# Kernel optimization log

Measured on AMD Instinct MI355X. Metric: run time of the kernel, lower is better.

Reference implementation:

```python
import jax, jax.numpy as jnp
import numpy as np

V = 8000; TZ = 128; TU = 256; B = 64; H = 1024; E = 512; DG = 64
GI = E + 2 * H + DG  # GRU input size = embed + z_ctx + u_ctx + degree


def _build_sparse_z(rng):
    # faithful vectorized version of get_sparse_selective_input (minus vocab SLOT branch)
    z_np = rng.integers(0, V + 10, size=(TZ, B))  # some ids >= V -> OOV copy path
    res = np.full((TZ, B, V + TZ), 1e-10, np.float32)
    w = z_np[:-1]                                   # [TZ-1, B]
    cond = (w == 2) | (w >= V)
    ti, bi = np.meshgrid(np.arange(TZ - 1), np.arange(B), indexing='ij')
    col = np.where(cond, V + ti, w)
    val = np.where(cond, np.float32(5.0), np.float32(1.0))
    res[ti + 1, bi, col] = val
    return jnp.asarray(res.transpose(1, 0, 2))      # [B, TZ, V+TZ]


def setup_inputs():
    key = jax.random.key(0)
    ks = jax.random.split(key, 16)
    s = 0.02
    iv = 1.0 / np.sqrt(H)
    return dict(
        z_enc_out=jax.random.normal(ks[0], (TZ, B, H), jnp.float32),
        u_enc_out=jax.random.normal(ks[1], (TU, B, H), jnp.float32),
        m_t_input=jax.random.randint(ks[2], (1, B), 0, V),
        degree_input=jax.random.normal(ks[3], (B, DG), jnp.float32),
        last_hidden=jax.random.normal(ks[4], (1, B, H), jnp.float32),
        sparse_z_input=_build_sparse_z(np.random.default_rng(0)),
        emb_W=jax.random.normal(ks[5], (V, E), jnp.float32) * s,
        attn_z_W=jax.random.normal(ks[6], (H, 2 * H), jnp.float32) * s,
        attn_z_b=jnp.zeros((H,), jnp.float32),
        attn_z_v=jax.random.normal(ks[7], (H,), jnp.float32) * iv,
        attn_u_W=jax.random.normal(ks[8], (H, 2 * H), jnp.float32) * s,
        attn_u_b=jnp.zeros((H,), jnp.float32),
        attn_u_v=jax.random.normal(ks[9], (H,), jnp.float32) * iv,
        gru_Wih=jax.random.normal(ks[10], (3 * H, GI), jnp.float32) * s,
        gru_Whh=jax.random.normal(ks[11], (3 * H, H), jnp.float32) * s,
        gru_bih=jnp.zeros((3 * H,), jnp.float32),
        gru_bhh=jnp.zeros((3 * H,), jnp.float32),
        proj_W=jax.random.normal(ks[12], (V, 3 * H), jnp.float32) * s,
        proj_b=jnp.zeros((V,), jnp.float32),
        copy2_W=jax.random.normal(ks[13], (H, H), jnp.float32) * s,
        copy2_b=jnp.zeros((H,), jnp.float32),
    )


def _attn(hidden, enc, W, b, v):
    # hidden [1,B,H], enc [T,B,H] -> context [1,B,H] (Bahdanau additive attention)
    enc_b = jnp.transpose(enc, (1, 0, 2))                       # [B,T,H]
    Hrep = jnp.broadcast_to(jnp.transpose(hidden, (1, 0, 2)), enc_b.shape)
    energy = jnp.tanh(jnp.concatenate([Hrep, enc_b], -1) @ W.T + b)  # [B,T,H]
    scores = jnp.einsum('bth,h->bt', energy, v)[:, None, :]    # [B,1,T]
    alpha = jax.nn.softmax(scores, axis=2)
    ctx = jnp.einsum('bit,bth->bih', alpha, enc_b)              # [B,1,H]
    return jnp.transpose(ctx, (1, 0, 2))                        # [1,B,H]


def _gru_step(x, h, Wih, Whh, bih, bhh):
    # single step, torch gate order (r, z, n)
    gi = x @ Wih.T + bih
    gh = h @ Whh.T + bhh
    ir, iz, inn = jnp.split(gi, 3, -1)
    hr, hz, hn = jnp.split(gh, 3, -1)
    r = jax.nn.sigmoid(ir + hr)
    z = jax.nn.sigmoid(iz + hz)
    n = jnp.tanh(inn + r * hn)
    return (1.0 - z) * n + z * h


def reference(z_enc_out, u_enc_out, m_t_input, degree_input, last_hidden,
              sparse_z_input, emb_W, attn_z_W, attn_z_b, attn_z_v,
              attn_u_W, attn_u_b, attn_u_v, gru_Wih, gru_Whh, gru_bih, gru_bhh,
              proj_W, proj_b, copy2_W, copy2_b):
    m_embed = emb_W[m_t_input]                                  # [1,B,E]
    z_ctx = _attn(last_hidden, z_enc_out, attn_z_W, attn_z_b, attn_z_v)  # [1,B,H]
    u_ctx = _attn(last_hidden, u_enc_out, attn_u_W, attn_u_b, attn_u_v)  # [1,B,H]
    gru_in = jnp.concatenate([m_embed, u_ctx, z_ctx, degree_input[None]], axis=2)
    gru_out = _gru_step(gru_in, last_hidden, gru_Wih, gru_Whh, gru_bih, gru_bhh)
    new_hidden = gru_out                                        # single-layer GRU, 1 step
    gen_score = (jnp.concatenate([z_ctx, u_ctx, gru_out], 2) @ proj_W.T + proj_b)[0]  # [B,V]
    # pointer copy scores over z encoder states
    z_cs = jnp.tanh(jnp.transpose(z_enc_out, (1, 0, 2)) @ copy2_W.T + copy2_b)  # [B,TZ,H]
    z_cs = jnp.einsum('bth,bh->bt', z_cs, gru_out[0])           # [B,TZ]
    m = jnp.max(z_cs, axis=1, keepdims=True)
    e = jnp.exp(z_cs - m)
    z_copy = jnp.log(jnp.einsum('bt,btv->bv', e, sparse_z_input)) + m  # [B,V+TZ]
    scores = jax.nn.softmax(jnp.concatenate([gen_score, z_copy], axis=1), axis=1)
    gen_s, zc = scores[:, :V], scores[:, V:]
    proba = jnp.concatenate([gen_s + zc[:, :V], zc[:, V:]], axis=1)  # [B, V+TZ]
    return (proba, new_hidden, gru_out)
```

## Files before the change

kernel.cpp:

```cpp
#include <hip/hip_runtime.h>
#include <cmath>

#define B64 64
#define H 1024
#define E 512
#define DG 64
#define GIN 2624
#define TZ 128
#define TU 256
#define V 8000
#define VT 8128
#define NC 16128

using bf16x8 = __attribute__((ext_vector_type(8))) short;
using f32x4  = __attribute__((ext_vector_type(4))) float;

__device__ inline unsigned pack2(float a, float b) {
    unsigned ua = __float_as_uint(a) + 0x8000u;
    unsigned ub = __float_as_uint(b) + 0x8000u;
    return __builtin_amdgcn_perm(ub, ua, 0x07060302u);
}
__device__ inline uint2 pack4(float4 v) {
    return make_uint2(pack2(v.x, v.y), pack2(v.z, v.w));
}

__device__ inline float fast_tanh(float x) {
    float e = __expf(2.f * x);
    return 1.f - 2.f / (e + 1.f);
}
__device__ inline float fast_sig(float x) {
    return 1.f / (1.f + __expf(-x));
}

__device__ inline void gl_lds16(const void* gptr, void* lptr) {
    __builtin_amdgcn_global_load_lds(
        (const __attribute__((address_space(1))) void*)gptr,
        (__attribute__((address_space(3))) void*)lptr, 16, 0, 0);
}

__global__ void k_cvt_all(const float* __restrict__ u_enc, const float* __restrict__ z_enc,
                          const float* __restrict__ azW, const float* __restrict__ auW,
                          const float* __restrict__ c2W,
                          unsigned short* __restrict__ ubf, unsigned short* __restrict__ zbf,
                          unsigned short* __restrict__ azWbf, unsigned short* __restrict__ auWbf,
                          unsigned short* __restrict__ c2Wbf)
{
    int n = blockIdx.x, k4 = threadIdx.x * 4;
    const float* src; unsigned short* dst; int ld, koff, r;
    if (n < 16384)      { src = u_enc; dst = ubf;   ld = 1024; koff = 0;    r = n; }
    else if (n < 24576) { src = z_enc; dst = zbf;   ld = 1024; koff = 0;    r = n - 16384; }
    else if (n < 25600) { src = azW;   dst = azWbf; ld = 2048; koff = 1024; r = n - 24576; }
    else if (n < 26624) { src = auW;   dst = auWbf; ld = 2048; koff = 1024; r = n - 25600; }
    else                { src = c2W;   dst = c2Wbf; ld = 1024; koff = 0;    r = n - 26624; }
    float4 v = *(const float4*)(src + (size_t)r * ld + koff + k4);
    *(uint2*)(dst + (size_t)r * 1024 + k4) = pack4(v);
}

__global__ __launch_bounds__(256) void fused_tanh_dot_bf(
    const unsigned short* __restrict__ A,
    const unsigned short* __restrict__ W,
    const float* __restrict__ addv, int add_stride,
    const float* __restrict__ multv, int mult_stride,
    float* __restrict__ outs)
{
    __shared__ unsigned short As[128 * 32];
    __shared__ unsigned short Bs[128 * 32];
    const int tid  = threadIdx.x;
    const int wave = tid >> 6, lane = tid & 63;
    const int wm = wave >> 1, wn = wave & 1;
    const int q = lane >> 4, l16 = lane & 15;
    const int m0 = blockIdx.x * 128;
    const int n0 = blockIdx.y * 128;
    const int lrow = lane >> 2;
    const int lk   = (lane & 3) * 8;

    f32x4 acc[4][4];
#pragma unroll
    for (int i = 0; i < 4; ++i)
#pragma unroll
        for (int j = 0; j < 4; ++j) acc[i][j] = f32x4{0.f, 0.f, 0.f, 0.f};

    for (int kt = 0; kt < 32; ++kt) {
        const int k0 = kt * 32;
        __syncthreads();
#pragma unroll
        for (int j = 0; j < 2; ++j) {
            int r0 = (wave * 2 + j) * 16;
            gl_lds16(A + (size_t)(m0 + r0 + lrow) * 1024 + k0 + lk, &As[r0 * 32]);
            gl_lds16(W + (size_t)(n0 + r0 + lrow) * 1024 + k0 + lk, &Bs[r0 * 32]);
        }
        __syncthreads();
        bf16x8 af[4], bfr[4];
#pragma unroll
        for (int t = 0; t < 4; ++t) af[t]  = *(bf16x8*)&As[(wm * 64 + t * 16 + l16) * 32 + q * 8];
#pragma unroll
        for (int t = 0; t < 4; ++t) bfr[t] = *(bf16x8*)&Bs[(wn * 64 + t * 16 + l16) * 32 + q * 8];
#pragma unroll
        for (int tm = 0; tm < 4; ++tm)
#pragma unroll
            for (int tn = 0; tn < 4; ++tn)
                acc[tm][tn] = __builtin_amdgcn_mfma_f32_16x16x32_bf16(
                    af[tm], bfr[tn], acc[tm][tn], 0, 0, 0);
    }

#pragma unroll
    for (int tm = 0; tm < 4; ++tm) {
#pragma unroll
        for (int r = 0; r < 4; ++r) {
            int R = m0 + wm * 64 + tm * 16 + q * 4 + r;
            int b = R & 63;
            float s = 0.f;
#pragma unroll
            for (int tn = 0; tn < 4; ++tn) {
                int col = n0 + wn * 64 + tn * 16 + l16;
                float e = acc[tm][tn][r] + addv[(size_t)b * add_stride + col];
                s += fast_tanh(e) * multv[(size_t)b * mult_stride + col];
            }
            s += __shfl_xor(s, 1);
            s += __shfl_xor(s, 2);
            s += __shfl_xor(s, 4);
            s += __shfl_xor(s, 8);
            if (l16 == 0) atomicAdd(&outs[R], s);
        }
    }
}

__global__ __launch_bounds__(256) void ftd_z_combo(
    const unsigned short* __restrict__ A,
    const unsigned short* __restrict__ Wz,
    const float* __restrict__ hbz, const float* __restrict__ azv,
    float* __restrict__ scores,
    const unsigned short* __restrict__ Wc,
    const float* __restrict__ c2b,
    float* __restrict__ tz)
{
    __shared__ unsigned short As[128 * 32];
    __shared__ unsigned short Bs[128 * 32];
    const int tid  = threadIdx.x;
    const int wave = tid >> 6, lane = tid & 63;
    const int wm = wave >> 1, wn = wave & 1;
    const int q = lane >> 4, l16 = lane & 15;
    const int m0 = blockIdx.x * 128;
    const bool isz = blockIdx.y < 8;
    const int n0 = (isz ? blockIdx.y : blockIdx.y - 8) * 128;
    const unsigned short* W = isz ? Wz : Wc;
    const int lrow = lane >> 2;
    const int lk   = (lane & 3) * 8;

    f32x4 acc[4][4];
#pragma unroll
    for (int i = 0; i < 4; ++i)
#pragma unroll
        for (int j = 0; j < 4; ++j) acc[i][j] = f32x4{0.f, 0.f, 0.f, 0.f};

    for (int kt = 0; kt < 32; ++kt) {
        const int k0 = kt * 32;
        __syncthreads();
#pragma unroll
        for (int j = 0; j < 2; ++j) {
            int r0 = (wave * 2 + j) * 16;
            gl_lds16(A + (size_t)(m0 + r0 + lrow) * 1024 + k0 + lk, &As[r0 * 32]);
            gl_lds16(W + (size_t)(n0 + r0 + lrow) * 1024 + k0 + lk, &Bs[r0 * 32]);
        }
        __syncthreads();
        bf16x8 af[4], bfr[4];
#pragma unroll
        for (int t = 0; t < 4; ++t) af[t]  = *(bf16x8*)&As[(wm * 64 + t * 16 + l16) * 32 + q * 8];
#pragma unroll
        for (int t = 0; t < 4; ++t) bfr[t] = *(bf16x8*)&Bs[(wn * 64 + t * 16 + l16) * 32 + q * 8];
#pragma unroll
        for (int tm = 0; tm < 4; ++tm)
#pragma unroll
            for (int tn = 0; tn < 4; ++tn)
                acc[tm][tn] = __builtin_amdgcn_mfma_f32_16x16x32_bf16(
                    af[tm], bfr[tn], acc[tm][tn], 0, 0, 0);
    }

    if (isz) {
#pragma unroll
        for (int tm = 0; tm < 4; ++tm) {
#pragma unroll
            for (int r = 0; r < 4; ++r) {
                int R = m0 + wm * 64 + tm * 16 + q * 4 + r;
                int b = R & 63;
                float s = 0.f;
#pragma unroll
                for (int tn = 0; tn < 4; ++tn) {
                    int col = n0 + wn * 64 + tn * 16 + l16;
                    float e = acc[tm][tn][r] + hbz[(size_t)b * 1024 + col];
                    s += fast_tanh(e) * azv[col];
                }
                s += __shfl_xor(s, 1);
                s += __shfl_xor(s, 2);
                s += __shfl_xor(s, 4);
                s += __shfl_xor(s, 8);
                if (l16 == 0) atomicAdd(&scores[R], s);
            }
        }
    } else {
#pragma unroll
        for (int tm = 0; tm < 4; ++tm) {
#pragma unroll
            for (int r = 0; r < 4; ++r) {
                int R = m0 + wm * 64 + tm * 16 + q * 4 + r;
#pragma unroll
                for (int tn = 0; tn < 4; ++tn) {
                    int col = n0 + wn * 64 + tn * 16 + l16;
                    tz[(size_t)R * 1024 + col] = fast_tanh(acc[tm][tn][r] + c2b[col]);
                }
            }
        }
    }
}

__global__ __launch_bounds__(256) void gemm_bt_mfma(
    const float* __restrict__ A, int lda,
    const float* __restrict__ W, int ldw, int koff,
    const float* __restrict__ bias,
    float* __restrict__ C, int N,
    int ks_total, int ks_chunk)
{
    __shared__ short As[64][40];
    __shared__ short Bs[64][40];
    const int tid  = threadIdx.x;
    const int wave = tid >> 6, lane = tid & 63;
    const int wm = wave >> 1, wn = wave & 1;
    const int q = lane >> 4, l16 = lane & 15;
    const int n0 = blockIdx.x * 64;
    const int kb = blockIdx.y * ks_chunk;
    const int ke = min(kb + ks_chunk, ks_total);

    f32x4 acc[2][2];
#pragma unroll
    for (int i = 0; i < 2; ++i)
#pragma unroll
        for (int j = 0; j < 2; ++j) acc[i][j] = f32x4{0.f, 0.f, 0.f, 0.f};

    for (int ks = kb; ks < ke; ++ks) {
        const int k0 = ks * 32;
        __syncthreads();
#pragma unroll
        for (int i = 0; i < 2; ++i) {
            int slot = i * 256 + tid;
            int row  = slot >> 3;
            int kq   = (slot & 7) << 2;
            float4 a = *(const float4*)(A + (size_t)row * lda + k0 + kq);
            *(uint2*)&As[row][kq] = pack4(a);
            float4 w = *(const float4*)(W + (size_t)(n0 + row) * ldw + koff + k0 + kq);
            *(uint2*)&Bs[row][kq] = pack4(w);
        }
        __syncthreads();
        bf16x8 af[2], bfr[2];
#pragma unroll
        for (int t = 0; t < 2; ++t) af[t]  = *(bf16x8*)&As[wm * 32 + t * 16 + l16][q * 8];
#pragma unroll
        for (int t = 0; t < 2; ++t) bfr[t] = *(bf16x8*)&Bs[wn * 32 + t * 16 + l16][q * 8];
#pragma unroll
        for (int tm = 0; tm < 2; ++tm)
#pragma unroll
            for (int tn = 0; tn < 2; ++tn)
                acc[tm][tn] = __builtin_amdgcn_mfma_f32_16x16x32_bf16(
                    af[tm], bfr[tn], acc[tm][tn], 0, 0, 0);
    }

#pragma unroll
    for (int tm = 0; tm < 2; ++tm) {
#pragma unroll
        for (int r = 0; r < 4; ++r) {
            int b = wm * 32 + tm * 16 + q * 4 + r;
#pragma unroll
            for (int tn = 0; tn < 2; ++tn) {
                int n = n0 + wn * 32 + tn * 16 + l16;
                float v = acc[tm][tn][r];
                if (blockIdx.y == 0) v += bias[n];
                atomicAdd(&C[(size_t)b * N + n], v);
            }
        }
    }
}

__global__ void k_gather(const int* __restrict__ mt, const float* __restrict__ embW,
                         const float* __restrict__ degree, float* __restrict__ x)
{
    int b = blockIdx.x, tid = threadIdx.x;
    int m = mt[b];
    for (int k = tid; k < E; k += 128) x[(size_t)b * GIN + k] = embW[(size_t)m * E + k];
    if (tid < DG) x[(size_t)b * GIN + E + 2 * H + tid] = degree[b * DG + tid];
}

__global__ __launch_bounds__(256) void k_softmax_ctx_bf(
    const float* __restrict__ scores, const unsigned short* __restrict__ encbf, int T,
    float* __restrict__ x, int xoff, float* __restrict__ y, int yoff)
{
    __shared__ float red[256];
    __shared__ float al[256];
    int b = blockIdx.x, hc = blockIdx.y, tid = threadIdx.x;
    float s = (tid < T) ? scores[tid * B64 + b] : -1e30f;
    red[tid] = s; __syncthreads();
    for (int off = 128; off > 0; off >>= 1) {
        if (tid < off) red[tid] = fmaxf(red[tid], red[tid + off]);
        __syncthreads();
    }
    float mx = red[0]; __syncthreads();
    float e = (tid < T) ? __expf(s - mx) : 0.f;
    red[tid] = e; __syncthreads();
    for (int off = 128; off > 0; off >>= 1) {
        if (tid < off) red[tid] += red[tid + off];
        __syncthreads();
    }
    float inv = 1.f / red[0];
    al[tid] = e * inv;
    __syncthreads();
    int h = hc * 512 + tid * 2;
    float a0 = 0.f, a1 = 0.f;
#pragma unroll 4
    for (int t = 0; t < T; ++t) {
        unsigned u = *(const unsigned*)(encbf + ((size_t)t * B64 + b) * 1024 + h);
        float w = al[t];
        a0 += w * __uint_as_float(u << 16);
        a1 += w * __uint_as_float(u & 0xffff0000u);
    }
    x[(size_t)b * GIN + xoff + h]     = a0;
    x[(size_t)b * GIN + xoff + h + 1] = a1;
    y[(size_t)b * 3072 + yoff + h]     = a0;
    y[(size_t)b * 3072 + yoff + h + 1] = a1;
}

__global__ void k_gate(const float* __restrict__ gi, const float* __restrict__ gh,
                       const float* __restrict__ h0, float* __restrict__ gru,
                       float* __restrict__ y, float* __restrict__ out_hid,
                       float* __restrict__ out_gru)
{
    int b = blockIdx.x, tid = threadIdx.x;
    for (int j = tid; j < H; j += 256) {
        float ir = gi[(size_t)b * 3072 + j];
        float iz = gi[(size_t)b * 3072 + H + j];
        float in_ = gi[(size_t)b * 3072 + 2 * H + j];
        float hr = gh[(size_t)b * 3072 + j];
        float hz = gh[(size_t)b * 3072 + H + j];
        float hn = gh[(size_t)b * 3072 + 2 * H + j];
        float r = fast_sig(ir + hr);
        float z = fast_sig(iz + hz);
        float n = fast_tanh(in_ + r * hn);
        float h = h0[(size_t)b * H + j];
        float o = (1.f - z) * n + z * h;
        gru[(size_t)b * H + j] = o;
        y[(size_t)b * 3072 + 2 * H + j] = o;
        out_hid[(size_t)b * H + j] = o;
        out_gru[(size_t)b * H + j] = o;
    }
}

__global__ __launch_bounds__(512) void k_zcs_dot(
    const float* __restrict__ tz, const float* __restrict__ gru,
    float* __restrict__ zraw)
{
    __shared__ float g[1024];
    int b = blockIdx.x, quarter = blockIdx.y, tid = threadIdx.x;
    int wave = tid >> 6, lane = tid & 63;
    for (int i = tid; i < 1024; i += 512) g[i] = gru[(size_t)b * 1024 + i];
    __syncthreads();
    float gr[16];
#pragma unroll
    for (int j = 0; j < 16; ++j) gr[j] = g[lane * 16 + j];
    int t0 = quarter * 32;
#pragma unroll
    for (int i = 0; i < 4; ++i) {
        int t = t0 + wave + i * 8;
        const float* row = tz + ((size_t)t * B64 + b) * 1024 + lane * 16;
        float s = 0.f;
#pragma unroll
        for (int c = 0; c < 4; ++c) {
            float4 v = *(const float4*)(row + c * 4);
            s += v.x * gr[c * 4 + 0] + v.y * gr[c * 4 + 1]
               + v.z * gr[c * 4 + 2] + v.w * gr[c * 4 + 3];
        }
#pragma unroll
        for (int off = 32; off > 0; off >>= 1) s += __shfl_xor(s, off);
        if (lane == 0) zraw[b * TZ + t] = s;
    }
}

__global__ void k_expw(const float* __restrict__ zraw,
                       float* __restrict__ ew, float* __restrict__ mb)
{
    __shared__ float r2[2];
    int b = blockIdx.x, tid = threadIdx.x;
    float s = zraw[b * TZ + tid];
    float m = s;
#pragma unroll
    for (int off = 32; off > 0; off >>= 1) m = fmaxf(m, __shfl_xor(m, off));
    if ((tid & 63) == 0) r2[tid >> 6] = m;
    __syncthreads();
    m = fmaxf(r2[0], r2[1]);
    ew[b * TZ + tid] = __expf(s - m);
    if (tid == 0) mb[b] = m;
}

__global__ __launch_bounds__(256) void k_sparse(
    const float* __restrict__ sz, const float* __restrict__ ew,
    const float* __restrict__ mb, float* __restrict__ zcopy)
{
    __shared__ float es[TZ];
    int c = blockIdx.x, b = blockIdx.y, tid = threadIdx.x;
    if (tid < TZ) es[tid] = ew[b * TZ + tid];
    __syncthreads();
    if (tid >= 254) return;
    int v4 = c * 254 + tid;
    const f32x4* base = (const f32x4*)(sz + (size_t)b * TZ * VT);
    float4 acc = make_float4(0.f, 0.f, 0.f, 0.f);
#pragma unroll 16
    for (int t = 0; t < TZ; ++t) {
        f32x4 xv = __builtin_nontemporal_load(&base[(size_t)t * (VT / 4) + v4]);
        float e = es[t];
        acc.x += e * xv[0]; acc.y += e * xv[1]; acc.z += e * xv[2]; acc.w += e * xv[3];
    }
    float m = mb[b];
    int v = v4 * 4;
    zcopy[(size_t)b * VT + v + 0] = __logf(acc.x) + m;
    zcopy[(size_t)b * VT + v + 1] = __logf(acc.y) + m;
    zcopy[(size_t)b * VT + v + 2] = __logf(acc.z) + m;
    zcopy[(size_t)b * VT + v + 3] = __logf(acc.w) + m;
}

__global__ __launch_bounds__(1024) void k_final(
    const float* __restrict__ gen, const float* __restrict__ zcopy,
    float* __restrict__ proba)
{
    __shared__ float lg[NC];
    __shared__ float wred[16];
    int b = blockIdx.x, tid = threadIdx.x;
    int lane = tid & 63, wave = tid >> 6;
    for (int i = tid; i < V; i += 1024) lg[i] = gen[(size_t)b * V + i];
    for (int i = tid; i < VT; i += 1024) lg[V + i] = zcopy[(size_t)b * VT + i];
    __syncthreads();
    float mx = -1e30f;
    for (int i = tid; i < NC; i += 1024) mx = fmaxf(mx, lg[i]);
#pragma unroll
    for (int off = 32; off > 0; off >>= 1) mx = fmaxf(mx, __shfl_xor(mx, off));
    if (lane == 0) wred[wave] = mx;
    __syncthreads();
    mx = wred[0];
#pragma unroll
    for (int w = 1; w < 16; ++w) mx = fmaxf(mx, wred[w]);
    __syncthreads();
    float sm = 0.f;
    for (int i = tid; i < NC; i += 1024) sm += __expf(lg[i] - mx);
#pragma unroll
    for (int off = 32; off > 0; off >>= 1) sm += __shfl_xor(sm, off);
    if (lane == 0) wred[wave] = sm;
    __syncthreads();
    float Z = 0.f;
#pragma unroll
    for (int w = 0; w < 16; ++w) Z += wred[w];
    float invZ = 1.f / Z;
    for (int v = tid; v < VT; v += 1024) {
        float p = __expf(lg[V + v] - mx) * invZ;
        if (v < V) p += __expf(lg[v] - mx) * invZ;
        proba[(size_t)b * VT + v] = p;
    }
}

extern "C" void kernel_launch(void* const* d_in, const int* in_sizes, int n_in,
                              void* d_out, int out_size, void* d_ws, size_t ws_size,
                              hipStream_t stream)
{
    const float* z_enc  = (const float*)d_in[0];
    const float* u_enc  = (const float*)d_in[1];
    const int*   mt     = (const int*)d_in[2];
    const float* degree = (const float*)d_in[3];
    const float* h0     = (const float*)d_in[4];
    const float* sz     = (const float*)d_in[5];
    const float* embW   = (const float*)d_in[6];
    const float* azW    = (const float*)d_in[7];
    const float* azb    = (const float*)d_in[8];
    const float* azv    = (const float*)d_in[9];
    const float* auW    = (const float*)d_in[10];
    const float* aub    = (const float*)d_in[11];
    const float* auv    = (const float*)d_in[12];
    const float* Wih    = (const float*)d_in[13];
    const float* Whh    = (const float*)d_in[14];
    const float* bih    = (const float*)d_in[15];
    const float* bhh    = (const float*)d_in[16];
    const float* pW     = (const float*)d_in[17];
    const float* pb     = (const float*)d_in[18];
    const float* c2W    = (const float*)d_in[19];
    const float* c2b    = (const float*)d_in[20];

    float* ws       = (float*)d_ws;
    float* scores_z = ws;
    float* scores_u = ws + 8192;
    float* hbz      = ws + 32768;
    float* hbu      = ws + 98304;
    float* gi       = ws + 163840;
    float* gh       = ws + 360448;
    float* gen      = ws + 557056;
    float* x        = ws + 1069056;
    float* y        = ws + 1236992;
    float* gru      = ws + 1433600;
    float* ew       = ws + 1499136;
    float* mb       = ws + 1507328;
    float* zcopy    = ws + 1507392;
    float* tz       = ws + 2027584;
    unsigned short* ubf   = (unsigned short*)(ws + 2027584 + 8388608);
    unsigned short* zbf   = ubf + (size_t)16384 * 1024;
    unsigned short* azWbf = zbf + (size_t)8192 * 1024;
    unsigned short* auWbf = azWbf + (size_t)1024 * 1024;
    unsigned short* c2Wbf = auWbf + (size_t)1024 * 1024;
    float* zraw = ws + 24571968;

    float* out_proba = (float*)d_out;
    float* out_hid   = out_proba + (size_t)B64 * VT;
    float* out_gru   = out_hid + (size_t)B64 * H;

    hipMemsetAsync(ws, 0, 1069056 * sizeof(float), stream);

    k_cvt_all<<<27648, 256, 0, stream>>>(u_enc, z_enc, azW, auW, c2W,
                                         ubf, zbf, azWbf, auWbf, c2Wbf);

    gemm_bt_mfma<<<dim3(16, 8), 256, 0, stream>>>(h0, 1024, azW, 2048, 0, azb, hbz, 1024, 32, 4);
    gemm_bt_mfma<<<dim3(16, 8), 256, 0, stream>>>(h0, 1024, auW, 2048, 0, aub, hbu, 1024, 32, 4);
    k_gather<<<64, 128, 0, stream>>>(mt, embW, degree, x);
    gemm_bt_mfma<<<dim3(48, 8), 256, 0, stream>>>(h0, 1024, Whh, 1024, 0, bhh, gh, 3072, 32, 4);

    ftd_z_combo<<<dim3(64, 16), 256, 0, stream>>>(zbf, azWbf, hbz, azv, scores_z,
                                                  c2Wbf, c2b, tz);
    fused_tanh_dot_bf<<<dim3(128, 8), 256, 0, stream>>>(ubf, auWbf, hbu, 1024, auv, 0, scores_u);

    k_softmax_ctx_bf<<<dim3(64, 2), 256, 0, stream>>>(scores_z, zbf, TZ, x, 1536, y, 0);
    k_softmax_ctx_bf<<<dim3(64, 2), 256, 0, stream>>>(scores_u, ubf, TU, x, 512, y, 1024);

    gemm_bt_mfma<<<dim3(48, 8), 256, 0, stream>>>(x, GIN, Wih, GIN, 0, bih, gi, 3072, 82, 11);
    k_gate<<<64, 256, 0, stream>>>(gi, gh, h0, gru, y, out_hid, out_gru);

    k_zcs_dot<<<dim3(64, 4), 512, 0, stream>>>(tz, gru, zraw);
    k_expw<<<64, 128, 0, stream>>>(zraw, ew, mb);

    gemm_bt_mfma<<<dim3(125, 8), 256, 0, stream>>>(y, 3072, pW, 3072, 0, pb, gen, 8000, 96, 12);

    k_sparse<<<dim3(8, 64), 256, 0, stream>>>(sz, ew, mb, zcopy);

    k_final<<<64, 1024, 0, stream>>>(gen, zcopy, out_proba);
}
```

Baseline: 806.7 us.

## Merge small kernels into fewer launches across gather, gemms, attention and softmax

Several small kernels are folded together: the embedding gather joins the bf16 conversion kernel, the three hidden-state GEMMs become one launch, the z/u/copy tanh-dot kernels become one grid, both softmax-context calls share one launch, and the exp/max step moves into the sparse kernel. This cuts launch overhead and lets independent work fill the GPU at the same time. In exchange each k_sparse block recomputes the row max and exponentials, and the merged kernels add a little branching.

```diff
diff --git a/kernel.cpp b/kernel.cpp
--- a/kernel.cpp
+++ b/kernel.cpp
@@ -43,9 +43,19 @@
                           const float* __restrict__ c2W,
                           unsigned short* __restrict__ ubf, unsigned short* __restrict__ zbf,
                           unsigned short* __restrict__ azWbf, unsigned short* __restrict__ auWbf,
-                          unsigned short* __restrict__ c2Wbf)
-{
-    int n = blockIdx.x, k4 = threadIdx.x * 4;
+                          unsigned short* __restrict__ c2Wbf,
+                          const int* __restrict__ mt, const float* __restrict__ embW,
+                          const float* __restrict__ degree, float* __restrict__ x)
+{
+    int n = blockIdx.x, tid = threadIdx.x;
+    if (n >= 27648) {
+        int b = n - 27648;
+        int m = mt[b];
+        for (int k = tid; k < E; k += 256) x[(size_t)b * GIN + k] = embW[(size_t)m * E + k];
+        if (tid < DG) x[(size_t)b * GIN + E + 2 * H + tid] = degree[b * DG + tid];
+        return;
+    }
+    int k4 = tid * 4;
     const float* src; unsigned short* dst; int ld, koff, r;
     if (n < 16384)      { src = u_enc; dst = ubf;   ld = 1024; koff = 0;    r = n; }
     else if (n < 24576) { src = z_enc; dst = zbf;   ld = 1024; koff = 0;    r = n - 16384; }
@@ -56,12 +66,15 @@
     *(uint2*)(dst + (size_t)r * 1024 + k4) = pack4(v);
 }
 
-__global__ __launch_bounds__(256) void fused_tanh_dot_bf(
-    const unsigned short* __restrict__ A,
-    const unsigned short* __restrict__ W,
-    const float* __restrict__ addv, int add_stride,
-    const float* __restrict__ multv, int mult_stride,
-    float* __restrict__ outs)
+__global__ __launch_bounds__(256) void ftd_all(
+    const unsigned short* __restrict__ zbf_, const unsigned short* __restrict__ ubf_,
+    const unsigned short* __restrict__ azWbf, const unsigned short* __restrict__ auWbf,
+    const unsigned short* __restrict__ c2Wbf,
+    const float* __restrict__ hbz, const float* __restrict__ hbu,
+    const float* __restrict__ azv, const float* __restrict__ auv,
+    const float* __restrict__ c2b,
+    float* __restrict__ scores_z, float* __restrict__ scores_u,
+    float* __restrict__ tz)
 {
     __shared__ unsigned short As[128 * 32];
     __shared__ unsigned short Bs[128 * 32];
@@ -69,10 +82,28 @@
     const int wave = tid >> 6, lane = tid & 63;
     const int wm = wave >> 1, wn = wave & 1;
     const int q = lane >> 4, l16 = lane & 15;
-    const int m0 = blockIdx.x * 128;
-    const int n0 = blockIdx.y * 128;
     const int lrow = lane >> 2;
     const int lk   = (lane & 3) * 8;
+
+    const int gid = blockIdx.x;
+    const bool isU = gid >= 1024;
+    int m0, n0;
+    const unsigned short *A, *W;
+    bool isTZ = false;
+    const float* addv; const float* vvec; float* outs;
+    if (isU) {
+        int g = gid - 1024;
+        m0 = (g & 127) * 128;
+        n0 = (g >> 7) * 128;
+        A = ubf_; W = auWbf;
+        addv = hbu; vvec = auv; outs = scores_u;
+    } else {
+        m0 = (gid & 63) * 128;
+        int by = gid >> 6;
+        A = zbf_;
+        if (by < 8) { n0 = by * 128; W = azWbf; addv = hbz; vvec = azv; outs = scores_z; }
+        else        { n0 = (by - 8) * 128; W = c2Wbf; isTZ = true; addv = nullptr; vvec = nullptr; outs = nullptr; }
+    }
 
     f32x4 acc[4][4];
 #pragma unroll
@@ -103,80 +134,7 @@
                     af[tm], bfr[tn], acc[tm][tn], 0, 0, 0);
     }
 
-#pragma unroll
-    for (int tm = 0; tm < 4; ++tm) {
-#pragma unroll
-        for (int r = 0; r < 4; ++r) {
-            int R = m0 + wm * 64 + tm * 16 + q * 4 + r;
-            int b = R & 63;
-            float s = 0.f;
-#pragma unroll
-            for (int tn = 0; tn < 4; ++tn) {
-                int col = n0 + wn * 64 + tn * 16 + l16;
-                float e = acc[tm][tn][r] + addv[(size_t)b * add_stride + col];
-                s += fast_tanh(e) * multv[(size_t)b * mult_stride + col];
-            }
-            s += __shfl_xor(s, 1);
-            s += __shfl_xor(s, 2);
-            s += __shfl_xor(s, 4);
-            s += __shfl_xor(s, 8);
-            if (l16 == 0) atomicAdd(&outs[R], s);
-        }
-    }
-}
-
-__global__ __launch_bounds__(256) void ftd_z_combo(
-    const unsigned short* __restrict__ A,
-    const unsigned short* __restrict__ Wz,
-    const float* __restrict__ hbz, const float* __restrict__ azv,
-    float* __restrict__ scores,
-    const unsigned short* __restrict__ Wc,
-    const float* __restrict__ c2b,
-    float* __restrict__ tz)
-{
-    __shared__ unsigned short As[128 * 32];
-    __shared__ unsigned short Bs[128 * 32];
-    const int tid  = threadIdx.x;
-    const int wave = tid >> 6, lane = tid & 63;
-    const int wm = wave >> 1, wn = wave & 1;
-    const int q = lane >> 4, l16 = lane & 15;
-    const int m0 = blockIdx.x * 128;
-    const bool isz = blockIdx.y < 8;
-    const int n0 = (isz ? blockIdx.y : blockIdx.y - 8) * 128;
-    const unsigned short* W = isz ? Wz : Wc;
-    const int lrow = lane >> 2;
-    const int lk   = (lane & 3) * 8;
-
-    f32x4 acc[4][4];
-#pragma unroll
-    for (int i = 0; i < 4; ++i)
-#pragma unroll
-        for (int j = 0; j < 4; ++j) acc[i][j] = f32x4{0.f, 0.f, 0.f, 0.f};
-
-    for (int kt = 0; kt < 32; ++kt) {
-        const int k0 = kt * 32;
-        __syncthreads();
-#pragma unroll
-        for (int j = 0; j < 2; ++j) {
-            int r0 = (wave * 2 + j) * 16;
-            gl_lds16(A + (size_t)(m0 + r0 + lrow) * 1024 + k0 + lk, &As[r0 * 32]);
-            gl_lds16(W + (size_t)(n0 + r0 + lrow) * 1024 + k0 + lk, &Bs[r0 * 32]);
-        }
-        __syncthreads();
-        bf16x8 af[4], bfr[4];
-#pragma unroll
-        for (int t = 0; t < 4; ++t) af[t]  = *(bf16x8*)&As[(wm * 64 + t * 16 + l16) * 32 + q * 8];
-#pragma unroll
-        for (int t = 0; t < 4; ++t) bfr[t] = *(bf16x8*)&Bs[(wn * 64 + t * 16 + l16) * 32 + q * 8];
-#pragma unroll
-        for (int tm = 0; tm < 4; ++tm)
-#pragma unroll
-            for (int tn = 0; tn < 4; ++tn)
-                acc[tm][tn] = __builtin_amdgcn_mfma_f32_16x16x32_bf16(
-                    af[tm], bfr[tn], acc[tm][tn], 0, 0, 0);
-    }
-
-    if (isz) {
+    if (!isTZ) {
 #pragma unroll
         for (int tm = 0; tm < 4; ++tm) {
 #pragma unroll
@@ -187,14 +145,14 @@
 #pragma unroll
                 for (int tn = 0; tn < 4; ++tn) {
                     int col = n0 + wn * 64 + tn * 16 + l16;
-                    float e = acc[tm][tn][r] + hbz[(size_t)b * 1024 + col];
-                    s += fast_tanh(e) * azv[col];
+                    float e = acc[tm][tn][r] + addv[(size_t)b * 1024 + col];
+                    s += fast_tanh(e) * vvec[col];
                 }
                 s += __shfl_xor(s, 1);
                 s += __shfl_xor(s, 2);
                 s += __shfl_xor(s, 4);
                 s += __shfl_xor(s, 8);
-                if (l16 == 0) atomicAdd(&scores[R], s);
+                if (l16 == 0) atomicAdd(&outs[R], s);
             }
         }
     } else {
@@ -213,22 +171,17 @@
     }
 }
 
-__global__ __launch_bounds__(256) void gemm_bt_mfma(
+__device__ __forceinline__ void gemm_core(
+    short (*As)[40], short (*Bs)[40], int tid,
     const float* __restrict__ A, int lda,
     const float* __restrict__ W, int ldw, int koff,
     const float* __restrict__ bias,
     float* __restrict__ C, int N,
-    int ks_total, int ks_chunk)
-{
-    __shared__ short As[64][40];
-    __shared__ short Bs[64][40];
-    const int tid  = threadIdx.x;
+    int n0, int kb, int ke, bool addbias)
+{
     const int wave = tid >> 6, lane = tid & 63;
     const int wm = wave >> 1, wn = wave & 1;
     const int q = lane >> 4, l16 = lane & 15;
-    const int n0 = blockIdx.x * 64;
-    const int kb = blockIdx.y * ks_chunk;
-    const int ke = min(kb + ks_chunk, ks_total);
 
     f32x4 acc[2][2];
 #pragma unroll
@@ -272,29 +225,61 @@
             for (int tn = 0; tn < 2; ++tn) {
                 int n = n0 + wn * 32 + tn * 16 + l16;
                 float v = acc[tm][tn][r];
-                if (blockIdx.y == 0) v += bias[n];
+                if (addbias) v += bias[n];
                 atomicAdd(&C[(size_t)b * N + n], v);
             }
         }
     }
 }
 
-__global__ void k_gather(const int* __restrict__ mt, const float* __restrict__ embW,
-                         const float* __restrict__ degree, float* __restrict__ x)
-{
-    int b = blockIdx.x, tid = threadIdx.x;
-    int m = mt[b];
-    for (int k = tid; k < E; k += 128) x[(size_t)b * GIN + k] = embW[(size_t)m * E + k];
-    if (tid < DG) x[(size_t)b * GIN + E + 2 * H + tid] = degree[b * DG + tid];
+__global__ __launch_bounds__(256) void gemm_bt_mfma(
+    const float* __restrict__ A, int lda,
+    const float* __restrict__ W, int ldw, int koff,
+    const float* __restrict__ bias,
+    float* __restrict__ C, int N,
+    int ks_total, int ks_chunk)
+{
+    __shared__ short As[64][40];
+    __shared__ short Bs[64][40];
+    int n0 = blockIdx.x * 64;
+    int kb = blockIdx.y * ks_chunk;
+    int ke = min(kb + ks_chunk, ks_total);
+    gemm_core(As, Bs, threadIdx.x, A, lda, W, ldw, koff, bias, C, N,
+              n0, kb, ke, blockIdx.y == 0);
+}
+
+__global__ __launch_bounds__(256) void gemm3(
+    const float* __restrict__ h0,
+    const float* __restrict__ azW, const float* __restrict__ azb, float* __restrict__ hbz,
+    const float* __restrict__ auW, const float* __restrict__ aub, float* __restrict__ hbu,
+    const float* __restrict__ Whh, const float* __restrict__ bhh, float* __restrict__ gh)
+{
+    __shared__ short As[64][40];
+    __shared__ short Bs[64][40];
+    int n = blockIdx.x;
+    const float *W, *bias; float* C; int ldw, N, n0, kc;
+    if (n < 128)      { W = azW; bias = azb; C = hbz; ldw = 2048; N = 1024; n0 = (n & 15) * 64;  kc = n >> 4; }
+    else if (n < 256) { n -= 128; W = auW; bias = aub; C = hbu; ldw = 2048; N = 1024; n0 = (n & 15) * 64; kc = n >> 4; }
+    else              { n -= 256; W = Whh; bias = bhh; C = gh;  ldw = 1024; N = 3072; n0 = (n % 48) * 64; kc = n / 48; }
+    int kb = kc * 4, ke = kb + 4;
+    gemm_core(As, Bs, threadIdx.x, h0, 1024, W, ldw, 0, bias, C, N, n0, kb, ke, kc == 0);
 }
 
 __global__ __launch_bounds__(256) void k_softmax_ctx_bf(
-    const float* __restrict__ scores, const unsigned short* __restrict__ encbf, int T,
-    float* __restrict__ x, int xoff, float* __restrict__ y, int yoff)
+    const float* __restrict__ scores_z, const float* __restrict__ scores_u,
+    const unsigned short* __restrict__ zbf_, const unsigned short* __restrict__ ubf_,
+    float* __restrict__ x, float* __restrict__ y)
 {
     __shared__ float red[256];
     __shared__ float al[256];
-    int b = blockIdx.x, hc = blockIdx.y, tid = threadIdx.x;
+    int b = blockIdx.x, tid = threadIdx.x;
+    int side = blockIdx.y >> 1, hc = blockIdx.y & 1;
+    const float* scores = side ? scores_u : scores_z;
+    const unsigned short* encbf = side ? ubf_ : zbf_;
+    int T = side ? TU : TZ;
+    int xoff = side ? 512 : 1536;
+    int yoff = side ? 1024 : 0;
+
     float s = (tid < T) ? scores[tid * B64 + b] : -1e30f;
     red[tid] = s; __syncthreads();
     for (int off = 128; off > 0; off >>= 1) {
@@ -381,29 +366,24 @@
     }
 }
 
-__global__ void k_expw(const float* __restrict__ zraw,
-                       float* __restrict__ ew, float* __restrict__ mb)
-{
-    __shared__ float r2[2];
-    int b = blockIdx.x, tid = threadIdx.x;
-    float s = zraw[b * TZ + tid];
-    float m = s;
-#pragma unroll
-    for (int off = 32; off > 0; off >>= 1) m = fmaxf(m, __shfl_xor(m, off));
-    if ((tid & 63) == 0) r2[tid >> 6] = m;
-    __syncthreads();
-    m = fmaxf(r2[0], r2[1]);
-    ew[b * TZ + tid] = __expf(s - m);
-    if (tid == 0) mb[b] = m;
-}
-
 __global__ __launch_bounds__(256) void k_sparse(
-    const float* __restrict__ sz, const float* __restrict__ ew,
-    const float* __restrict__ mb, float* __restrict__ zcopy)
+    const float* __restrict__ sz, const float* __restrict__ zraw,
+    float* __restrict__ zcopy)
 {
     __shared__ float es[TZ];
+    __shared__ float mred[2];
     int c = blockIdx.x, b = blockIdx.y, tid = threadIdx.x;
-    if (tid < TZ) es[tid] = ew[b * TZ + tid];
+    float sv = 0.f;
+    if (tid < TZ) {
+        sv = zraw[b * TZ + tid];
+        float mm = sv;
+#pragma unroll
+        for (int off = 32; off > 0; off >>= 1) mm = fmaxf(mm, __shfl_xor(mm, off));
+        if ((tid & 63) == 0) mred[tid >> 6] = mm;
+    }
+    __syncthreads();
+    float m = fmaxf(mred[0], mred[1]);
+    if (tid < TZ) es[tid] = __expf(sv - m);
     __syncthreads();
     if (tid >= 254) return;
     int v4 = c * 254 + tid;
@@ -415,7 +395,6 @@
         float e = es[t];
         acc.x += e * xv[0]; acc.y += e * xv[1]; acc.z += e * xv[2]; acc.w += e * xv[3];
     }
-    float m = mb[b];
     int v = v4 * 4;
     zcopy[(size_t)b * VT + v + 0] = __logf(acc.x) + m;
     zcopy[(size_t)b * VT + v + 1] = __logf(acc.y) + m;
@@ -498,8 +477,6 @@
     float* x        = ws + 1069056;
     float* y        = ws + 1236992;
     float* gru      = ws + 1433600;
-    float* ew       = ws + 1499136;
-    float* mb       = ws + 1507328;
     float* zcopy    = ws + 1507392;
     float* tz       = ws + 2027584;
     unsigned short* ubf   = (unsigned short*)(ws + 2027584 + 8388608);
@@ -515,30 +492,26 @@
 
     hipMemsetAsync(ws, 0, 1069056 * sizeof(float), stream);
 
-    k_cvt_all<<<27648, 256, 0, stream>>>(u_enc, z_enc, azW, auW, c2W,
-                                         ubf, zbf, azWbf, auWbf, c2Wbf);
-
-    gemm_bt_mfma<<<dim3(16, 8), 256, 0, stream>>>(h0, 1024, azW, 2048, 0, azb, hbz, 1024, 32, 4);
-    gemm_bt_mfma<<<dim3(16, 8), 256, 0, stream>>>(h0, 1024, auW, 2048, 0, aub, hbu, 1024, 32, 4);
-    k_gather<<<64, 128, 0, stream>>>(mt, embW, degree, x);
-    gemm_bt_mfma<<<dim3(48, 8), 256, 0, stream>>>(h0, 1024, Whh, 1024, 0, bhh, gh, 3072, 32, 4);
-
-    ftd_z_combo<<<dim3(64, 16), 256, 0, stream>>>(zbf, azWbf, hbz, azv, scores_z,
-                                                  c2Wbf, c2b, tz);
-    fused_tanh_dot_bf<<<dim3(128, 8), 256, 0, stream>>>(ubf, auWbf, hbu, 1024, auv, 0, scores_u);
-
-    k_softmax_ctx_bf<<<dim3(64, 2), 256, 0, stream>>>(scores_z, zbf, TZ, x, 1536, y, 0);
-    k_softmax_ctx_bf<<<dim3(64, 2), 256, 0, stream>>>(scores_u, ubf, TU, x, 512, y, 1024);
+    k_cvt_all<<<27712, 256, 0, stream>>>(u_enc, z_enc, azW, auW, c2W,
+                                         ubf, zbf, azWbf, auWbf, c2Wbf,
+                                         mt, embW, degree, x);
+
+    gemm3<<<640, 256, 0, stream>>>(h0, azW, azb, hbz, auW, aub, hbu, Whh, bhh, gh);
+
+    ftd_all<<<2048, 256, 0, stream>>>(zbf, ubf, azWbf, auWbf, c2Wbf,
+                                      hbz, hbu, azv, auv, c2b,
+                                      scores_z, scores_u, tz);
+
+    k_softmax_ctx_bf<<<dim3(64, 4), 256, 0, stream>>>(scores_z, scores_u, zbf, ubf, x, y);
 
     gemm_bt_mfma<<<dim3(48, 8), 256, 0, stream>>>(x, GIN, Wih, GIN, 0, bih, gi, 3072, 82, 11);
     k_gate<<<64, 256, 0, stream>>>(gi, gh, h0, gru, y, out_hid, out_gru);
 
     k_zcs_dot<<<dim3(64, 4), 512, 0, stream>>>(tz, gru, zraw);
-    k_expw<<<64, 128, 0, stream>>>(zraw, ew, mb);
 
     gemm_bt_mfma<<<dim3(125, 8), 256, 0, stream>>>(y, 3072, pW, 3072, 0, pb, gen, 8000, 96, 12);
 
-    k_sparse<<<dim3(8, 64), 256, 0, stream>>>(sz, ew, mb, zcopy);
+    k_sparse<<<dim3(8, 64), 256, 0, stream>>>(sz, zraw, zcopy);
 
     k_final<<<64, 1024, 0, stream>>>(gen, zcopy, out_proba);
 }
```

Result: faster. 770.3 us (-4.5%).
